# Optimization experiments

Hardware: AMD Instinct MI355X
Metric: run time of the kernel (lower is better)

The kernel has to match this reference:

```python
import jax, jax.numpy as jnp
import numpy as np

B = 256          # batch
IMG = 28         # img_width
K = 9            # kernel_size
NUM_CLASSES = 10
NUM_ITER = 3
NUM_ROUTE = 32 * 6 * 6  # 1152


def _conv(x, w, b, stride):
    # x: [B,C,H,W], w: [O,I,K,K] (OIHW), VALID padding as in nn.Conv2d(padding=0)
    y = jax.lax.conv_general_dilated(x, w, (stride, stride), 'VALID',
                                     dimension_numbers=('NCHW', 'OIHW', 'NCHW'))
    return y + b[None, :, None, None]


def _squash(t, axis=-1):
    sq = jnp.sum(t * t, axis=axis, keepdims=True)
    return (sq / (1.0 + sq)) * t / jnp.sqrt(sq)


def setup_inputs() -> dict:
    key = jax.random.key(0)
    ks = jax.random.split(key, 10)
    rn = lambda k, s, sc=0.05: jax.random.normal(k, s, dtype=jnp.float32) * sc
    return {
        'x': jax.random.uniform(ks[0], (B, 1, IMG, IMG), dtype=jnp.float32),
        'conv1_w': rn(ks[1], (256, 1, K, K)),
        'conv1_b': jnp.zeros((256,), jnp.float32),
        # 8 primary-capsule convs of 32 channels stacked as one 256-out conv
        'prim_w': rn(ks[2], (8 * 32, 256, K, K)),
        'prim_b': jnp.zeros((8 * 32,), jnp.float32),
        # torch.randn init, std 1, shape [num_capsules, num_route_nodes, in, out]
        'route_w': jax.random.normal(ks[3], (NUM_CLASSES, NUM_ROUTE, 8, 16), dtype=jnp.float32),
        'dec_w1': rn(ks[4], (16 * NUM_CLASSES, 512)),
        'dec_b1': jnp.zeros((512,), jnp.float32),
        'dec_w2': rn(ks[5], (512, 1024)),
        'dec_b2': jnp.zeros((1024,), jnp.float32),
        'dec_w3': rn(ks[6], (1024, IMG * IMG)),
        'dec_b3': jnp.zeros((IMG * IMG,), jnp.float32),
    }


def reference(x, conv1_w, conv1_b, prim_w, prim_b, route_w,
              dec_w1, dec_b1, dec_w2, dec_b2, dec_w3, dec_b3):
    b = x.shape[0]
    # conv1 + relu: [B,256,20,20]
    h = jax.nn.relu(_conv(x, conv1_w, conv1_b, 1))
    # primary capsules: [B,8*32,6,6] -> [B,1152,8] (capsule c flattens its own 32x6x6 block)
    p = _conv(h, prim_w, prim_b, 2)
    p = p.reshape(b, 8, -1).transpose(0, 2, 1)
    p = _squash(p)  # squash over the 8-dim capsule vectors
    # priors: [10,B,1152,1,16]
    priors = jnp.einsum('bri,crio->cbro', p, route_w)[:, :, :, None, :]
    logits = jnp.zeros_like(priors)
    outputs = None
    for i in range(NUM_ITER):
        probs = jax.nn.softmax(logits, axis=2)            # over route nodes
        outputs = _squash(jnp.sum(probs * priors, axis=2, keepdims=True))  # [10,B,1,1,16]
        if i != NUM_ITER - 1:
            logits = logits + jnp.sum(priors * outputs, axis=-1, keepdims=True)
    v = outputs.reshape(NUM_CLASSES, b, 16).transpose(1, 0, 2)  # [B,10,16]
    classes = jax.nn.softmax(jnp.sqrt(jnp.sum(v * v, axis=-1)), axis=1)  # [B,10]
    # y is None path: one-hot of argmax class
    y = jax.nn.one_hot(jnp.argmax(classes, axis=1), NUM_CLASSES, dtype=v.dtype)
    masked = (v * y[:, :, None]).reshape(b, -1)  # [B,160]
    h1 = jax.nn.relu(masked @ dec_w1 + dec_b1)
    h2 = jax.nn.relu(h1 @ dec_w2 + dec_b2)
    recon = jax.nn.sigmoid(h2 @ dec_w3 + dec_b3)  # [B,784]
    return classes, recon
```

## Files before the change

### kernel.cpp

```cpp
#include <hip/hip_runtime.h>
#include <hip/hip_bf16.h>
#include <math.h>

constexpr int BB = 256;
constexpr int NCLS = 10;
constexpr int NROUTE = 1152;

typedef __attribute__((ext_vector_type(8))) short s16x8;
typedef __attribute__((ext_vector_type(4))) float f32x4;

__device__ __forceinline__ void gl16(const void* g, void* l) {
  __builtin_amdgcn_global_load_lds(
      (const __attribute__((address_space(1))) void*)g,
      (__attribute__((address_space(3))) void*)l, 16, 0, 0);
}

__global__ __launch_bounds__(256) void k_conv1b(const float* __restrict__ x,
    const float* __restrict__ w, const float* __restrict__ bias,
    __hip_bfloat16* __restrict__ hT_hi, __hip_bfloat16* __restrict__ hT_lo,
    int b0) {
  int b_l = blockIdx.x >> 2, q = blockIdx.x & 3;
  __shared__ float sx[784];
  __shared__ float sw[64 * 81];
  int t = threadIdx.x;
  for (int i = t; i < 784; i += 256) sx[i] = x[(size_t)(b0 + b_l) * 784 + i];
  for (int i = t; i < 5184; i += 256) sw[i] = w[(size_t)q * 5184 + i];
  __syncthreads();
  int oc = q * 64 + (t & 63);
  int wv = t >> 6;
  float wreg[81];
#pragma unroll
  for (int k = 0; k < 81; ++k) wreg[k] = sw[(t & 63) * 81 + k];
  float bv = bias[oc];
  for (int st = wv * 10; st < wv * 10 + 10; ++st) {
    int y = st >> 1, x0 = (st & 1) * 10;
    float acc[10];
#pragma unroll
    for (int i = 0; i < 10; ++i) acc[i] = bv;
#pragma unroll
    for (int ky = 0; ky < 9; ++ky) {
      const float* row = &sx[(y + ky) * 28 + x0];
      float rv[18];
#pragma unroll
      for (int i = 0; i < 18; ++i) rv[i] = row[i];
#pragma unroll
      for (int kx = 0; kx < 9; ++kx) {
        float wgt = wreg[ky * 9 + kx];
#pragma unroll
        for (int xi = 0; xi < 10; ++xi) acc[xi] = fmaf(rv[kx + xi], wgt, acc[xi]);
      }
    }
#pragma unroll
    for (int xi = 0; xi < 10; ++xi) {
      float av = fmaxf(acc[xi], 0.f);
      __hip_bfloat16 hi = __float2bfloat16(av);
      float lo = av - __bfloat162float(hi);
      size_t idx = ((size_t)(b_l * 400 + y * 20 + x0 + xi)) * 256 + oc;
      hT_hi[idx] = hi;
      hT_lo[idx] = __float2bfloat16(lo);
    }
  }
}

__global__ __launch_bounds__(256) void k_cvtw(const float* __restrict__ w,
    __hip_bfloat16* __restrict__ wt_hi, __hip_bfloat16* __restrict__ wt_lo) {
  int oc = blockIdx.x >> 2, icq = blockIdx.x & 3;
  __shared__ float sw[5184];
  int t = threadIdx.x;
  const float* src = w + ((size_t)oc * 256 + icq * 64) * 81;
  for (int i = t; i < 5184; i += 256) sw[i] = src[i];
  __syncthreads();
  for (int i = t; i < 5184; i += 256) {
    int tap = i >> 6, icl = i & 63;
    float v = sw[icl * 81 + tap];
    __hip_bfloat16 hi = __float2bfloat16(v);
    float lo = v - __bfloat162float(hi);
    size_t dst = (size_t)tap * 65536 + (size_t)oc * 256 + icq * 64 + icl;
    wt_hi[dst] = hi;
    wt_lo[dst] = __float2bfloat16(lo);
  }
}

constexpr int PB_BUF = 32768;

__global__ __launch_bounds__(512, 2) void k_prim3(
    const __hip_bfloat16* __restrict__ hT_hi, const __hip_bfloat16* __restrict__ hT_lo,
    const __hip_bfloat16* __restrict__ wt_hi, const __hip_bfloat16* __restrict__ wt_lo,
    float* __restrict__ pout) {
  __shared__ __align__(16) char lds[2 * PB_BUF];
  int x = blockIdx.x & 7, g = blockIdx.x >> 3;
  int nM = (x < 4) ? 5 : 4;
  if (g >= nM * 6) return;
  int Mblk = x + (g / 6) * 8;
  int rem = g - (g / 6) * 6;
  int kb = rem % 3, Nblk = rem / 3;
  int m0 = Mblk * 128, oc0 = Nblk * 128;
  int t = threadIdx.x, wv = t >> 6, lane = t & 63;
  int jswz = (t & 3) ^ ((t >> 2) & 3);
  int rA = t >> 2;
  size_t roA;
  {
    int m = m0 + rA;
    int b = m / 36, s = m - b * 36, oy = s / 6, ox = s - oy * 6;
    roA = ((size_t)(b * 400 + oy * 40 + ox * 2)) * 512 + (size_t)(jswz * 16);
  }
  size_t boB = ((size_t)(oc0 + rA)) * 512 + (size_t)(jswz * 16);
  const char* hTh = (const char*)hT_hi;
  const char* hTl = (const char*)hT_lo;
  const char* wth = (const char*)wt_hi;
  const char* wtl = (const char*)wt_lo;

  auto stage = [&](int bufi, int s) {
    int tt = s >> 3, icc = s & 7;
    int tap = kb * 27 + tt;
    int ky = tap / 9, kx = tap - ky * 9;
    size_t offA = (size_t)((ky * 20 + kx) * 512 + icc * 64);
    size_t offB = (size_t)tap * 131072 + (size_t)(icc * 64);
    char* base = lds + bufi * PB_BUF + wv * 1024;
    gl16(hTh + roA + offA, base);
    gl16(hTl + roA + offA, base + 8192);
    gl16(wth + boB + offB, base + 16384);
    gl16(wtl + boB + offB, base + 24576);
  };

  int wr = wv >> 2, wc = wv & 3;
  int lr = lane & 15;
  int swz16 = ((lane >> 4) ^ (lane & 3)) * 16;
  int arow[4], brow[2];
#pragma unroll
  for (int i = 0; i < 4; ++i) arow[i] = (wr * 64 + i * 16 + lr) * 64 + swz16;
#pragma unroll
  for (int j = 0; j < 2; ++j) brow[j] = 16384 + (wc * 32 + j * 16 + lr) * 64 + swz16;

  f32x4 acc[4][2];
#pragma unroll
  for (int i = 0; i < 4; ++i)
#pragma unroll
    for (int j = 0; j < 2; ++j) acc[i][j] = (f32x4){0.f, 0.f, 0.f, 0.f};

  stage(0, 0);
  __syncthreads();
#pragma unroll 1
  for (int s = 0; s < 216; ++s) {
    int cur = s & 1;
    if (s + 1 < 216) stage(cur ^ 1, s + 1);
    const char* Ab = lds + cur * PB_BUF;
    s16x8 ah[4], al[4], bh[2], bl[2];
#pragma unroll
    for (int i = 0; i < 4; ++i) {
      ah[i] = *(const s16x8*)(Ab + arow[i]);
      al[i] = *(const s16x8*)(Ab + 8192 + arow[i]);
    }
#pragma unroll
    for (int j = 0; j < 2; ++j) {
      bh[j] = *(const s16x8*)(Ab + brow[j]);
      bl[j] = *(const s16x8*)(Ab + 8192 + brow[j]);
    }
#pragma unroll
    for (int i = 0; i < 4; ++i)
#pragma unroll
      for (int j = 0; j < 2; ++j) {
        acc[i][j] = __builtin_amdgcn_mfma_f32_16x16x32_bf16(ah[i], bh[j], acc[i][j], 0, 0, 0);
        acc[i][j] = __builtin_amdgcn_mfma_f32_16x16x32_bf16(ah[i], bl[j], acc[i][j], 0, 0, 0);
        acc[i][j] = __builtin_amdgcn_mfma_f32_16x16x32_bf16(al[i], bh[j], acc[i][j], 0, 0, 0);
      }
    __syncthreads();
  }
  float* pb = pout + (size_t)kb * (4608 * 256);
#pragma unroll
  for (int i = 0; i < 4; ++i)
#pragma unroll
    for (int j = 0; j < 2; ++j) {
      int n = oc0 + wc * 32 + j * 16 + lr;
#pragma unroll
      for (int qq = 0; qq < 4; ++qq) {
        int m = m0 + wr * 64 + i * 16 + (lane >> 4) * 4 + qq;
        pb[(size_t)m * 256 + n] = acc[i][j][qq];
      }
    }
}

__global__ __launch_bounds__(256) void k_squash2(const float* __restrict__ pout,
    const float* __restrict__ bias, float* __restrict__ psT, int b0) {
  int b_l = blockIdx.x;
  int t = threadIdx.x;
  __shared__ float buf[9216];
  __shared__ float sq[256];
  __shared__ float sc[32];
  float bv = bias[t];
  for (int s = 0; s < 36; ++s) {
    size_t base = ((size_t)(b_l * 36 + s)) * 256 + t;
    float val = pout[base] + pout[base + 1179648] + pout[base + 2359296] + bv;
    sq[t] = val * val;
    __syncthreads();
    if (t < 32) {
      float ss = 0.f;
#pragma unroll
      for (int i = 0; i < 8; ++i) ss += sq[t + i * 32];
      sc[t] = sqrtf(ss) / (1.f + ss);
    }
    __syncthreads();
    buf[t * 36 + s] = val * sc[t & 31];
    __syncthreads();
  }
  float* dst = psT + (size_t)(b0 + b_l) * 9216;
  for (int i = t; i < 9216; i += 256) dst[i] = buf[i];
}

__global__ __launch_bounds__(768) void k_route5(const float* __restrict__ psT,
    const float* __restrict__ rw, float* __restrict__ vout) {
  int c = blockIdx.x >> 8;
  int b = blockIdx.x & 255;
  int tid = threadIdx.x;
  int wave = tid >> 6, lane = tid & 63;
  int oh = lane >> 5;
  int rs = wave * 32 + (lane & 31);
  __shared__ float lredm[12];
  __shared__ float lreds[12];
  __shared__ float ored[12][2][8];
  __shared__ float osum[16];
  __shared__ float vsq[16];

  float pri[3][8];
  float lgr[3] = {0.f, 0.f, 0.f};
#pragma unroll
  for (int k = 0; k < 3; ++k)
#pragma unroll
    for (int j = 0; j < 8; ++j) pri[k][j] = 0.f;

#pragma unroll
  for (int k = 0; k < 3; ++k) {
    int r = rs + k * 384;
    const float* wr_ = &rw[((size_t)c * 1152 + r) * 128 + oh * 8];
    float ps8[8];
#pragma unroll
    for (int i = 0; i < 8; ++i) ps8[i] = psT[(size_t)b * 9216 + i * 1152 + r];
#pragma unroll
    for (int i = 0; i < 8; ++i) {
      float4 w0 = *(const float4*)&wr_[i * 16];
      float4 w1 = *(const float4*)&wr_[i * 16 + 4];
      float w8[8] = {w0.x, w0.y, w0.z, w0.w, w1.x, w1.y, w1.z, w1.w};
#pragma unroll
      for (int j = 0; j < 8; ++j) pri[k][j] = fmaf(ps8[i], w8[j], pri[k][j]);
    }
  }

  for (int it = 0; it < 3; ++it) {
    float a[8];
    if (it == 0) {
      const float invu = 1.f / 1152.f;
#pragma unroll
      for (int j = 0; j < 8; ++j)
        a[j] = (pri[0][j] + pri[1][j] + pri[2][j]) * invu;
    } else {
      float mx = fmaxf(fmaxf(lgr[0], lgr[1]), lgr[2]);
#pragma unroll
      for (int off = 16; off; off >>= 1) mx = fmaxf(mx, __shfl_xor(mx, off));
      if (lane == 0) lredm[wave] = mx;
      __syncthreads();
      mx = lredm[0];
      for (int w = 1; w < 12; ++w) mx = fmaxf(mx, lredm[w]);
      float er[3];
      float sm = 0.f;
#pragma unroll
      for (int k = 0; k < 3; ++k) {
        er[k] = expf(lgr[k] - mx);
        sm += er[k];
      }
#pragma unroll
      for (int off = 16; off; off >>= 1) sm += __shfl_xor(sm, off);
      if (lane == 0) lreds[wave] = sm;
      __syncthreads();
      float s = 0.f;
      for (int w = 0; w < 12; ++w) s += lreds[w];
      float inv = 1.f / s;
#pragma unroll
      for (int j = 0; j < 8; ++j) a[j] = 0.f;
#pragma unroll
      for (int k = 0; k < 3; ++k) {
        float p = er[k] * inv;
#pragma unroll
        for (int j = 0; j < 8; ++j) a[j] = fmaf(p, pri[k][j], a[j]);
      }
    }
#pragma unroll
    for (int off = 16; off; off >>= 1)
#pragma unroll
      for (int j = 0; j < 8; ++j) a[j] += __shfl_xor(a[j], off);
    if ((lane & 31) == 0) {
#pragma unroll
      for (int j = 0; j < 8; ++j) ored[wave][oh][j] = a[j];
    }
    __syncthreads();
    if (tid < 16) {
      float s = 0.f;
      for (int w = 0; w < 12; ++w) s += ored[w][tid >> 3][tid & 7];
      osum[tid] = s;
    }
    __syncthreads();
    if (tid < 16) {
      float sqv = 0.f;
#pragma unroll
      for (int o = 0; o < 16; ++o) sqv += osum[o] * osum[o];
      float sc = sqrtf(sqv) / (1.f + sqv);
      vsq[tid] = osum[tid] * sc;
    }
    __syncthreads();
    if (it < 2) {
      float vh[8];
#pragma unroll
      for (int j = 0; j < 8; ++j) vh[j] = vsq[oh * 8 + j];
#pragma unroll
      for (int k = 0; k < 3; ++k) {
        float d = 0.f;
#pragma unroll
        for (int j = 0; j < 8; ++j) d = fmaf(pri[k][j], vh[j], d);
        d += __shfl_xor(d, 32);
        lgr[k] += d;
      }
      __syncthreads();
    }
  }
  if (tid < 16) vout[((size_t)c * BB + b) * 16 + tid] = vsq[tid];
}

__global__ __launch_bounds__(64) void k_cls2(const float* __restrict__ v,
                                             float* __restrict__ classes,
                                             int* __restrict__ am,
                                             float* __restrict__ vsel) {
  int b = blockIdx.x;
  int t = threadIdx.x;
  __shared__ float snrm[10];
  __shared__ int samax;
  if (t < 10) {
    float sq = 0.f;
#pragma unroll
    for (int o = 0; o < 16; ++o) {
      float xx = v[(size_t)(t * BB + b) * 16 + o];
      sq += xx * xx;
    }
    snrm[t] = sqrtf(sq);
  }
  __syncthreads();
  if (t == 0) {
    int amx = 0;
    float bm = snrm[0];
    for (int cc = 1; cc < 10; ++cc)
      if (snrm[cc] > bm) { bm = snrm[cc]; amx = cc; }
    samax = amx;
    am[b] = amx;
  }
  __syncthreads();
  if (t < 10) {
    float mx = snrm[0];
    for (int cc = 1; cc < 10; ++cc) mx = fmaxf(mx, snrm[cc]);
    float sm = 0.f;
    for (int cc = 0; cc < 10; ++cc) sm += expf(snrm[cc] - mx);
    classes[b * 10 + t] = expf(snrm[t] - mx) / sm;
  }
  if (t < 16) vsel[b * 16 + t] = v[((size_t)samax * BB + b) * 16 + t];
}

__global__ __launch_bounds__(512) void k_fc1s(const float* __restrict__ vsel,
    const int* __restrict__ am, const float* __restrict__ w1,
    const float* __restrict__ b1, float* __restrict__ h1) {
  int b = blockIdx.x;
  int n = threadIdx.x;
  __shared__ float sv[16];
  __shared__ int sam;
  if (n < 16) sv[n] = vsel[b * 16 + n];
  if (n == 0) sam = am[b];
  __syncthreads();
  float acc = b1[n];
  int base = sam * 16;
#pragma unroll
  for (int i = 0; i < 16; ++i)
    acc = fmaf(sv[i], w1[(size_t)(base + i) * 512 + n], acc);
  h1[(size_t)b * 512 + n] = fmaxf(acc, 0.f);
}

template <int ACT>
__global__ __launch_bounds__(256) void k_fc32(const float* __restrict__ A,
                                              const float* __restrict__ W,
                                              const float* __restrict__ bias,
                                              float* __restrict__ O, int M,
                                              int N, int K) {
  int n0 = blockIdx.x * 32, m0 = blockIdx.y * 32;
  __shared__ float sa[32][33];
  __shared__ float sb[32][34];
  int tid = threadIdx.x, ty = tid >> 4, tx = tid & 15;
  float acc[2][2] = {};
  for (int k0 = 0; k0 < K; k0 += 32) {
    __syncthreads();
    for (int i = tid; i < 1024; i += 256) {
      int m = i >> 5, k = i & 31;
      sa[m][k] = A[(size_t)(m0 + m) * K + k0 + k];
      int kk = i >> 5, n = i & 31;
      int nn = n0 + n;
      sb[kk][n] = (nn < N) ? W[(size_t)(k0 + kk) * N + nn] : 0.f;
    }
    __syncthreads();
#pragma unroll
    for (int k = 0; k < 32; ++k) {
      float a0 = sa[ty * 2 + 0][k];
      float a1 = sa[ty * 2 + 1][k];
      float b0 = sb[k][tx * 2 + 0];
      float b1v = sb[k][tx * 2 + 1];
      acc[0][0] = fmaf(a0, b0, acc[0][0]);
      acc[0][1] = fmaf(a0, b1v, acc[0][1]);
      acc[1][0] = fmaf(a1, b0, acc[1][0]);
      acc[1][1] = fmaf(a1, b1v, acc[1][1]);
    }
  }
#pragma unroll
  for (int i = 0; i < 2; ++i) {
    int m = m0 + ty * 2 + i;
#pragma unroll
    for (int j = 0; j < 2; ++j) {
      int n = n0 + tx * 2 + j;
      if (n < N) {
        float xv = acc[i][j] + bias[n];
        if (ACT == 0)
          xv = fmaxf(xv, 0.f);
        else
          xv = 1.f / (1.f + expf(-xv));
        O[(size_t)m * N + n] = xv;
      }
    }
  }
}

extern "C" void kernel_launch(void* const* d_in, const int* in_sizes, int n_in,
                              void* d_out, int out_size, void* d_ws,
                              size_t ws_size, hipStream_t stream) {
  (void)in_sizes; (void)n_in; (void)out_size; (void)ws_size;
  const float* x       = (const float*)d_in[0];
  const float* conv1_w = (const float*)d_in[1];
  const float* conv1_b = (const float*)d_in[2];
  const float* prim_w  = (const float*)d_in[3];
  const float* prim_b  = (const float*)d_in[4];
  const float* route_w = (const float*)d_in[5];
  const float* dec_w1  = (const float*)d_in[6];
  const float* dec_b1  = (const float*)d_in[7];
  const float* dec_w2  = (const float*)d_in[8];
  const float* dec_b2  = (const float*)d_in[9];
  const float* dec_w3  = (const float*)d_in[10];
  const float* dec_b3  = (const float*)d_in[11];
  float* out = (float*)d_out;

  char* wsb = (char*)d_ws;
  __hip_bfloat16* hT_hi = (__hip_bfloat16*)(wsb);
  __hip_bfloat16* hT_lo = (__hip_bfloat16*)(wsb + 26214400);
  __hip_bfloat16* wt_hi = (__hip_bfloat16*)(wsb + 52428800);
  __hip_bfloat16* wt_lo = (__hip_bfloat16*)(wsb + 63045632);
  float* pout = (float*)(wsb + 73662464);
  float* psT  = (float*)(wsb + 87818240);
  float* v    = (float*)(wsb + 97255424);
  float* h1   = (float*)(wsb + 97419264);
  float* h2   = (float*)(wsb + 97943552);
  int*   am   = (int*)  (wsb + 98992128);
  float* vsel = (float*)(wsb + 98996224);

  k_cvtw<<<1024, 256, 0, stream>>>(prim_w, wt_hi, wt_lo);
  for (int hh = 0; hh < 2; ++hh) {
    int b0 = hh * 128;
    k_conv1b<<<512, 256, 0, stream>>>(x, conv1_w, conv1_b, hT_hi, hT_lo, b0);
    k_prim3<<<240, 512, 0, stream>>>(hT_hi, hT_lo, wt_hi, wt_lo, pout);
    k_squash2<<<128, 256, 0, stream>>>(pout, prim_b, psT, b0);
  }
  k_route5<<<2560, 768, 0, stream>>>(psT, route_w, v);
  k_cls2<<<256, 64, 0, stream>>>(v, out, am, vsel);
  k_fc1s<<<256, 512, 0, stream>>>(vsel, am, dec_w1, dec_b1, h1);
  k_fc32<0><<<dim3(32, 8), 256, 0, stream>>>(h1, dec_w2, dec_b2, h2, 256, 1024, 512);
  k_fc32<1><<<dim3(25, 8), 256, 0, stream>>>(h2, dec_w3, dec_b3, out + 2560, 256, 784, 1024);
}
```

Measured before the change: 792.6 us.

## Halve prim conv N-tile to 64 and store squashed capsules route-major

The primary-capsule GEMM now uses 128x64 output tiles instead of 128x128 and launches 480 blocks instead of 240, which spreads the work over more CUs. The B-operand staging is reorganised so half the threads load the hi weights and half the lo weights, and the LDS buffer shrinks to match. The squash kernel now writes psT in [b][route][8] order through a padded shared buffer, so the routing kernel can fetch each 8-vector with two float4 loads instead of eight strided loads. The smaller tile lowers A-operand reuse and adds more global traffic for A in exchange for better occupancy.

```diff
diff --git a/kernel.cpp b/kernel.cpp
--- a/kernel.cpp
+++ b/kernel.cpp
@@ -81,7 +81,7 @@
   }
 }
 
-constexpr int PB_BUF = 32768;
+constexpr int PB_BUF = 24576;
 
 __global__ __launch_bounds__(512, 2) void k_prim3(
     const __hip_bfloat16* __restrict__ hT_hi, const __hip_bfloat16* __restrict__ hT_lo,
@@ -90,11 +90,11 @@
   __shared__ __align__(16) char lds[2 * PB_BUF];
   int x = blockIdx.x & 7, g = blockIdx.x >> 3;
   int nM = (x < 4) ? 5 : 4;
-  if (g >= nM * 6) return;
-  int Mblk = x + (g / 6) * 8;
-  int rem = g - (g / 6) * 6;
+  if (g >= nM * 12) return;
+  int Mblk = x + (g / 12) * 8;
+  int rem = g % 12;
   int kb = rem % 3, Nblk = rem / 3;
-  int m0 = Mblk * 128, oc0 = Nblk * 128;
+  int m0 = Mblk * 128, oc0 = Nblk * 64;
   int t = threadIdx.x, wv = t >> 6, lane = t & 63;
   int jswz = (t & 3) ^ ((t >> 2) & 3);
   int rA = t >> 2;
@@ -104,11 +104,14 @@
     int b = m / 36, s = m - b * 36, oy = s / 6, ox = s - oy * 6;
     roA = ((size_t)(b * 400 + oy * 40 + ox * 2)) * 512 + (size_t)(jswz * 16);
   }
-  size_t boB = ((size_t)(oc0 + rA)) * 512 + (size_t)(jswz * 16);
+  int slotB = t & 255;
+  int rowB = slotB >> 2;
+  int jswzB = (slotB & 3) ^ (rowB & 3);
+  size_t boB = ((size_t)(oc0 + rowB)) * 512 + (size_t)(jswzB * 16);
   const char* hTh = (const char*)hT_hi;
   const char* hTl = (const char*)hT_lo;
-  const char* wth = (const char*)wt_hi;
-  const char* wtl = (const char*)wt_lo;
+  const char* srcB = (t < 256) ? (const char*)wt_hi : (const char*)wt_lo;
+  int dstBoff = 16384 + ((t >= 256) ? 4096 : 0) + (wv & 3) * 1024;
 
   auto stage = [&](int bufi, int s) {
     int tt = s >> 3, icc = s & 7;
@@ -116,25 +119,24 @@
     int ky = tap / 9, kx = tap - ky * 9;
     size_t offA = (size_t)((ky * 20 + kx) * 512 + icc * 64);
     size_t offB = (size_t)tap * 131072 + (size_t)(icc * 64);
-    char* base = lds + bufi * PB_BUF + wv * 1024;
-    gl16(hTh + roA + offA, base);
-    gl16(hTl + roA + offA, base + 8192);
-    gl16(wth + boB + offB, base + 16384);
-    gl16(wtl + boB + offB, base + 24576);
+    char* baseA = lds + bufi * PB_BUF + wv * 1024;
+    gl16(hTh + roA + offA, baseA);
+    gl16(hTl + roA + offA, baseA + 8192);
+    gl16(srcB + boB + offB, lds + bufi * PB_BUF + dstBoff);
   };
 
-  int wr = wv >> 2, wc = wv & 3;
+  int wr = wv >> 1, wc = wv & 1;
   int lr = lane & 15;
   int swz16 = ((lane >> 4) ^ (lane & 3)) * 16;
-  int arow[4], brow[2];
-#pragma unroll
-  for (int i = 0; i < 4; ++i) arow[i] = (wr * 64 + i * 16 + lr) * 64 + swz16;
+  int arow[2], brow[2];
+#pragma unroll
+  for (int i = 0; i < 2; ++i) arow[i] = (wr * 32 + i * 16 + lr) * 64 + swz16;
 #pragma unroll
   for (int j = 0; j < 2; ++j) brow[j] = 16384 + (wc * 32 + j * 16 + lr) * 64 + swz16;
 
-  f32x4 acc[4][2];
-#pragma unroll
-  for (int i = 0; i < 4; ++i)
+  f32x4 acc[2][2];
+#pragma unroll
+  for (int i = 0; i < 2; ++i)
 #pragma unroll
     for (int j = 0; j < 2; ++j) acc[i][j] = (f32x4){0.f, 0.f, 0.f, 0.f};
 
@@ -145,19 +147,19 @@
     int cur = s & 1;
     if (s + 1 < 216) stage(cur ^ 1, s + 1);
     const char* Ab = lds + cur * PB_BUF;
-    s16x8 ah[4], al[4], bh[2], bl[2];
-#pragma unroll
-    for (int i = 0; i < 4; ++i) {
+    s16x8 ah[2], al[2], bh[2], bl[2];
+#pragma unroll
+    for (int i = 0; i < 2; ++i) {
       ah[i] = *(const s16x8*)(Ab + arow[i]);
       al[i] = *(const s16x8*)(Ab + 8192 + arow[i]);
     }
 #pragma unroll
     for (int j = 0; j < 2; ++j) {
       bh[j] = *(const s16x8*)(Ab + brow[j]);
-      bl[j] = *(const s16x8*)(Ab + 8192 + brow[j]);
-    }
-#pragma unroll
-    for (int i = 0; i < 4; ++i)
+      bl[j] = *(const s16x8*)(Ab + 4096 + brow[j]);
+    }
+#pragma unroll
+    for (int i = 0; i < 2; ++i)
 #pragma unroll
       for (int j = 0; j < 2; ++j) {
         acc[i][j] = __builtin_amdgcn_mfma_f32_16x16x32_bf16(ah[i], bh[j], acc[i][j], 0, 0, 0);
@@ -168,13 +170,13 @@
   }
   float* pb = pout + (size_t)kb * (4608 * 256);
 #pragma unroll
-  for (int i = 0; i < 4; ++i)
+  for (int i = 0; i < 2; ++i)
 #pragma unroll
     for (int j = 0; j < 2; ++j) {
       int n = oc0 + wc * 32 + j * 16 + lr;
 #pragma unroll
       for (int qq = 0; qq < 4; ++qq) {
-        int m = m0 + wr * 64 + i * 16 + (lane >> 4) * 4 + qq;
+        int m = m0 + wr * 32 + i * 16 + (lane >> 4) * 4 + qq;
         pb[(size_t)m * 256 + n] = acc[i][j][qq];
       }
     }
@@ -184,10 +186,11 @@
     const float* __restrict__ bias, float* __restrict__ psT, int b0) {
   int b_l = blockIdx.x;
   int t = threadIdx.x;
-  __shared__ float buf[9216];
+  __shared__ float buf[32 * 289];
   __shared__ float sq[256];
   __shared__ float sc[32];
   float bv = bias[t];
+  int c32 = t & 31, ii = t >> 5;
   for (int s = 0; s < 36; ++s) {
     size_t base = ((size_t)(b_l * 36 + s)) * 256 + t;
     float val = pout[base] + pout[base + 1179648] + pout[base + 2359296] + bv;
@@ -200,11 +203,11 @@
       sc[t] = sqrtf(ss) / (1.f + ss);
     }
     __syncthreads();
-    buf[t * 36 + s] = val * sc[t & 31];
+    buf[c32 * 289 + s * 8 + ii] = val * sc[c32];
     __syncthreads();
   }
   float* dst = psT + (size_t)(b0 + b_l) * 9216;
-  for (int i = t; i < 9216; i += 256) dst[i] = buf[i];
+  for (int i = t; i < 9216; i += 256) dst[i] = buf[i + i / 288];
 }
 
 __global__ __launch_bounds__(768) void k_route5(const float* __restrict__ psT,
@@ -232,9 +235,9 @@
   for (int k = 0; k < 3; ++k) {
     int r = rs + k * 384;
     const float* wr_ = &rw[((size_t)c * 1152 + r) * 128 + oh * 8];
-    float ps8[8];
-#pragma unroll
-    for (int i = 0; i < 8; ++i) ps8[i] = psT[(size_t)b * 9216 + i * 1152 + r];
+    const float4* pp = (const float4*)&psT[((size_t)b * 1152 + r) * 8];
+    float4 pa = pp[0], pb4 = pp[1];
+    float ps8[8] = {pa.x, pa.y, pa.z, pa.w, pb4.x, pb4.y, pb4.z, pb4.w};
 #pragma unroll
     for (int i = 0; i < 8; ++i) {
       float4 w0 = *(const float4*)&wr_[i * 16];
@@ -465,7 +468,7 @@
   for (int hh = 0; hh < 2; ++hh) {
     int b0 = hh * 128;
     k_conv1b<<<512, 256, 0, stream>>>(x, conv1_w, conv1_b, hT_hi, hT_lo, b0);
-    k_prim3<<<240, 512, 0, stream>>>(hT_hi, hT_lo, wt_hi, wt_lo, pout);
+    k_prim3<<<480, 512, 0, stream>>>(hT_hi, hT_lo, wt_hi, wt_lo, pout);
     k_squash2<<<128, 256, 0, stream>>>(pout, prim_b, psT, b0);
   }
   k_route5<<<2560, 768, 0, stream>>>(psT, route_w, v);
```

Measured after the change: 795.6 us. Within noise of the previous version (+0.4%).

## Halve prim GEMM block threads, parallelize squash, and store capsule vectors contiguously

Applied to the files above, without the earlier changes.

The primary-capsule GEMM now runs 256 threads per block instead of 512. Each wave computes a 64x64 tile (4x4 MFMA accumulators), and each thread issues twice as many async global-to-LDS loads. This raises per-wave data reuse but uses more registers and leaves fewer waves to hide latency. The squash kernel is spread over a 36x128 grid with shuffle-based reductions in place of a serial 36-step loop, and it writes psT in route-major, 8-contiguous layout. The routing kernel then loads each capsule's 8 values with two float4 reads instead of 8 strided scalar loads.

```diff
diff --git a/kernel.cpp b/kernel.cpp
--- a/kernel.cpp
+++ b/kernel.cpp
@@ -81,30 +81,33 @@
   }
 }
 
-constexpr int PB_BUF = 32768;
-
-__global__ __launch_bounds__(512, 2) void k_prim3(
+constexpr int P4_BUF = 32768;
+
+__global__ __launch_bounds__(256) void k_prim4(
     const __hip_bfloat16* __restrict__ hT_hi, const __hip_bfloat16* __restrict__ hT_lo,
     const __hip_bfloat16* __restrict__ wt_hi, const __hip_bfloat16* __restrict__ wt_lo,
     float* __restrict__ pout) {
-  __shared__ __align__(16) char lds[2 * PB_BUF];
+  __shared__ __align__(16) char lds[2 * P4_BUF];
   int x = blockIdx.x & 7, g = blockIdx.x >> 3;
   int nM = (x < 4) ? 5 : 4;
   if (g >= nM * 6) return;
   int Mblk = x + (g / 6) * 8;
-  int rem = g - (g / 6) * 6;
+  int rem = g % 6;
   int kb = rem % 3, Nblk = rem / 3;
   int m0 = Mblk * 128, oc0 = Nblk * 128;
   int t = threadIdx.x, wv = t >> 6, lane = t & 63;
-  int jswz = (t & 3) ^ ((t >> 2) & 3);
+  int q = t & 3;
   int rA = t >> 2;
-  size_t roA;
+  int jswz = q ^ (rA & 3);
+  size_t roA0, roA1;
   {
-    int m = m0 + rA;
-    int b = m / 36, s = m - b * 36, oy = s / 6, ox = s - oy * 6;
-    roA = ((size_t)(b * 400 + oy * 40 + ox * 2)) * 512 + (size_t)(jswz * 16);
-  }
-  size_t boB = ((size_t)(oc0 + rA)) * 512 + (size_t)(jswz * 16);
+    int m = m0 + rA; int b = m / 36, s = m - b * 36, oy = s / 6, ox = s - oy * 6;
+    roA0 = ((size_t)(b * 400 + oy * 40 + ox * 2)) * 512 + (size_t)(jswz * 16);
+    m = m0 + rA + 64; b = m / 36; s = m - b * 36; oy = s / 6; ox = s - oy * 6;
+    roA1 = ((size_t)(b * 400 + oy * 40 + ox * 2)) * 512 + (size_t)(jswz * 16);
+  }
+  size_t boB0 = ((size_t)(oc0 + rA)) * 512 + (size_t)(jswz * 16);
+  size_t boB1 = ((size_t)(oc0 + rA + 64)) * 512 + (size_t)(jswz * 16);
   const char* hTh = (const char*)hT_hi;
   const char* hTl = (const char*)hT_lo;
   const char* wth = (const char*)wt_hi;
@@ -116,27 +119,31 @@
     int ky = tap / 9, kx = tap - ky * 9;
     size_t offA = (size_t)((ky * 20 + kx) * 512 + icc * 64);
     size_t offB = (size_t)tap * 131072 + (size_t)(icc * 64);
-    char* base = lds + bufi * PB_BUF + wv * 1024;
-    gl16(hTh + roA + offA, base);
-    gl16(hTl + roA + offA, base + 8192);
-    gl16(wth + boB + offB, base + 16384);
-    gl16(wtl + boB + offB, base + 24576);
+    char* d = lds + bufi * P4_BUF + t * 16;
+    gl16(hTh + roA0 + offA, d);
+    gl16(hTh + roA1 + offA, d + 4096);
+    gl16(hTl + roA0 + offA, d + 8192);
+    gl16(hTl + roA1 + offA, d + 12288);
+    gl16(wth + boB0 + offB, d + 16384);
+    gl16(wth + boB1 + offB, d + 20480);
+    gl16(wtl + boB0 + offB, d + 24576);
+    gl16(wtl + boB1 + offB, d + 28672);
   };
 
-  int wr = wv >> 2, wc = wv & 3;
+  int wr = wv >> 1, wc = wv & 1;
   int lr = lane & 15;
   int swz16 = ((lane >> 4) ^ (lane & 3)) * 16;
-  int arow[4], brow[2];
+  int arow[4], brow[4];
 #pragma unroll
   for (int i = 0; i < 4; ++i) arow[i] = (wr * 64 + i * 16 + lr) * 64 + swz16;
 #pragma unroll
-  for (int j = 0; j < 2; ++j) brow[j] = 16384 + (wc * 32 + j * 16 + lr) * 64 + swz16;
-
-  f32x4 acc[4][2];
+  for (int j = 0; j < 4; ++j) brow[j] = 16384 + (wc * 64 + j * 16 + lr) * 64 + swz16;
+
+  f32x4 acc[4][4];
 #pragma unroll
   for (int i = 0; i < 4; ++i)
 #pragma unroll
-    for (int j = 0; j < 2; ++j) acc[i][j] = (f32x4){0.f, 0.f, 0.f, 0.f};
+    for (int j = 0; j < 4; ++j) acc[i][j] = (f32x4){0.f, 0.f, 0.f, 0.f};
 
   stage(0, 0);
   __syncthreads();
@@ -144,22 +151,22 @@
   for (int s = 0; s < 216; ++s) {
     int cur = s & 1;
     if (s + 1 < 216) stage(cur ^ 1, s + 1);
-    const char* Ab = lds + cur * PB_BUF;
-    s16x8 ah[4], al[4], bh[2], bl[2];
+    const char* Ab = lds + cur * P4_BUF;
+    s16x8 ah[4], al[4], bh[4], bl[4];
 #pragma unroll
     for (int i = 0; i < 4; ++i) {
       ah[i] = *(const s16x8*)(Ab + arow[i]);
       al[i] = *(const s16x8*)(Ab + 8192 + arow[i]);
     }
 #pragma unroll
-    for (int j = 0; j < 2; ++j) {
+    for (int j = 0; j < 4; ++j) {
       bh[j] = *(const s16x8*)(Ab + brow[j]);
       bl[j] = *(const s16x8*)(Ab + 8192 + brow[j]);
     }
 #pragma unroll
     for (int i = 0; i < 4; ++i)
 #pragma unroll
-      for (int j = 0; j < 2; ++j) {
+      for (int j = 0; j < 4; ++j) {
         acc[i][j] = __builtin_amdgcn_mfma_f32_16x16x32_bf16(ah[i], bh[j], acc[i][j], 0, 0, 0);
         acc[i][j] = __builtin_amdgcn_mfma_f32_16x16x32_bf16(ah[i], bl[j], acc[i][j], 0, 0, 0);
         acc[i][j] = __builtin_amdgcn_mfma_f32_16x16x32_bf16(al[i], bh[j], acc[i][j], 0, 0, 0);
@@ -170,8 +177,8 @@
 #pragma unroll
   for (int i = 0; i < 4; ++i)
 #pragma unroll
-    for (int j = 0; j < 2; ++j) {
-      int n = oc0 + wc * 32 + j * 16 + lr;
+    for (int j = 0; j < 4; ++j) {
+      int n = oc0 + wc * 64 + j * 16 + lr;
 #pragma unroll
       for (int qq = 0; qq < 4; ++qq) {
         int m = m0 + wr * 64 + i * 16 + (lane >> 4) * 4 + qq;
@@ -180,31 +187,28 @@
     }
 }
 
-__global__ __launch_bounds__(256) void k_squash2(const float* __restrict__ pout,
+__global__ __launch_bounds__(256) void k_squash3(const float* __restrict__ pout,
     const float* __restrict__ bias, float* __restrict__ psT, int b0) {
-  int b_l = blockIdx.x;
+  int s = blockIdx.x;
+  int b_l = blockIdx.y;
   int t = threadIdx.x;
-  __shared__ float buf[9216];
-  __shared__ float sq[256];
-  __shared__ float sc[32];
-  float bv = bias[t];
-  for (int s = 0; s < 36; ++s) {
-    size_t base = ((size_t)(b_l * 36 + s)) * 256 + t;
-    float val = pout[base] + pout[base + 1179648] + pout[base + 2359296] + bv;
-    sq[t] = val * val;
-    __syncthreads();
-    if (t < 32) {
-      float ss = 0.f;
-#pragma unroll
-      for (int i = 0; i < 8; ++i) ss += sq[t + i * 32];
-      sc[t] = sqrtf(ss) / (1.f + ss);
-    }
-    __syncthreads();
-    buf[t * 36 + s] = val * sc[t & 31];
-    __syncthreads();
-  }
-  float* dst = psT + (size_t)(b0 + b_l) * 9216;
-  for (int i = t; i < 9216; i += 256) dst[i] = buf[i];
+  int c32 = t & 31;
+  __shared__ float ws[4][32];
+  __shared__ float buf2[256];
+  size_t base = ((size_t)(b_l * 36 + s)) * 256 + t;
+  float val = pout[base] + pout[base + 1179648] + pout[base + 2359296] + bias[t];
+  float v2 = val * val;
+  v2 += __shfl_xor(v2, 32);
+  int wvv = t >> 6, lane = t & 63;
+  if (lane < 32) ws[wvv][lane] = v2;
+  __syncthreads();
+  float ss = ws[0][c32] + ws[1][c32] + ws[2][c32] + ws[3][c32];
+  float sc = sqrtf(ss) / (1.f + ss);
+  buf2[t] = val * sc;
+  __syncthreads();
+  int cc = t >> 3, jj = t & 7;
+  psT[(size_t)(b0 + b_l) * 9216 + (size_t)cc * 288 + s * 8 + jj] =
+      buf2[jj * 32 + cc];
 }
 
 __global__ __launch_bounds__(768) void k_route5(const float* __restrict__ psT,
@@ -232,9 +236,9 @@
   for (int k = 0; k < 3; ++k) {
     int r = rs + k * 384;
     const float* wr_ = &rw[((size_t)c * 1152 + r) * 128 + oh * 8];
-    float ps8[8];
-#pragma unroll
-    for (int i = 0; i < 8; ++i) ps8[i] = psT[(size_t)b * 9216 + i * 1152 + r];
+    const float4* pp = (const float4*)&psT[((size_t)b * 1152 + r) * 8];
+    float4 pa = pp[0], pb4 = pp[1];
+    float ps8[8] = {pa.x, pa.y, pa.z, pa.w, pb4.x, pb4.y, pb4.z, pb4.w};
 #pragma unroll
     for (int i = 0; i < 8; ++i) {
       float4 w0 = *(const float4*)&wr_[i * 16];
@@ -465,8 +469,8 @@
   for (int hh = 0; hh < 2; ++hh) {
     int b0 = hh * 128;
     k_conv1b<<<512, 256, 0, stream>>>(x, conv1_w, conv1_b, hT_hi, hT_lo, b0);
-    k_prim3<<<240, 512, 0, stream>>>(hT_hi, hT_lo, wt_hi, wt_lo, pout);
-    k_squash2<<<128, 256, 0, stream>>>(pout, prim_b, psT, b0);
+    k_prim4<<<240, 256, 0, stream>>>(hT_hi, hT_lo, wt_hi, wt_lo, pout);
+    k_squash3<<<dim3(36, 128), 256, 0, stream>>>(pout, prim_b, psT, b0);
   }
   k_route5<<<2560, 768, 0, stream>>>(psT, route_w, v);
   k_cls2<<<256, 64, 0, stream>>>(v, out, am, vsel);
```

Result: no change. 792.7 us (+0.0%).
